# Performance work log

Hardware: AMD Instinct MI355X
Metric: run time of the kernel (lower is better)

## Reference

```python
import jax, jax.numpy as jnp
import numpy as np

MODES = (16, 16, 16)  # (kx, ky, kz); rfft keeps kz//2+1 = 9 modes on last axis


def setup_inputs() -> dict:
    key = jax.random.key(0)
    k_x, k_w1, k_w2 = jax.random.split(key, 3)
    B, C, H, W, D = 4, 64, 64, 64, 64
    hidden = C // 4
    kzr = MODES[2] // 2 + 1
    gate_dim = MODES[0] * MODES[1] * kzr  # 16*16*9 = 2304
    x = jax.random.normal(k_x, (B, C, H, W, D), dtype=jnp.float32)
    w1 = jax.random.normal(k_w1, (C, hidden), dtype=jnp.float32) * (1.0 / np.sqrt(C))
    b1 = jnp.zeros((hidden,), dtype=jnp.float32)
    w2 = jax.random.normal(k_w2, (hidden, gate_dim), dtype=jnp.float32) * (1.0 / np.sqrt(hidden))
    b2 = jnp.zeros((gate_dim,), dtype=jnp.float32)
    return {"x": x, "w1": w1, "b1": b1, "w2": w2, "b2": b2}


def reference(x, w1, b1, w2, b2):
    B = x.shape[0]
    kx, ky, kz = MODES
    kzr = kz // 2 + 1
    # Gate network: global average pool over spatial dims -> MLP -> sigmoid
    pooled = jnp.mean(x, axis=(2, 3, 4))                      # [B, C]
    h = jax.nn.relu(pooled @ w1 + b1)                          # [B, C//4]
    gates = jax.nn.sigmoid(h @ w2 + b2)                        # [B, kx*ky*kzr]
    gates = gates.reshape(B, 1, kx, ky, kzr)                   # broadcast over channels
    # Full 3D rFFT, gate only the low-frequency corner block, inverse FFT
    x_ft = jnp.fft.rfftn(x, axes=(-3, -2, -1))                 # [B, C, H, W, D//2+1] complex
    x_ft_gated = x_ft.at[:, :, :kx, :ky, :kzr].multiply(gates.astype(x_ft.real.dtype))
    out = jnp.fft.irfftn(x_ft_gated, s=x.shape[-3:], axes=(-3, -2, -1))
    return out.astype(x.dtype)
```

## Files before the change

kernel.cpp:

```cpp
#include <hip/hip_runtime.h>

namespace {

typedef float f2 __attribute__((ext_vector_type(2)));
typedef float vf4 __attribute__((ext_vector_type(4)));

__device__ __forceinline__ f2 mkf2(float a, float b) { f2 r; r.x = a; r.y = b; return r; }
__device__ __forceinline__ f2 pkfma(float s, f2 b, f2 c) {
  return __builtin_elementwise_fma(mkf2(s, s), b, c);
}

constexpr float COS64[64] = {
  1.00000000f,  0.99518473f,  0.98078528f,  0.95694034f,
  0.92387953f,  0.88192126f,  0.83146961f,  0.77301045f,
  0.70710678f,  0.63439328f,  0.55557023f,  0.47139674f,
  0.38268343f,  0.29028468f,  0.19509032f,  0.09801714f,
  0.00000000f, -0.09801714f, -0.19509032f, -0.29028468f,
 -0.38268343f, -0.47139674f, -0.55557023f, -0.63439328f,
 -0.70710678f, -0.77301045f, -0.83146961f, -0.88192126f,
 -0.92387953f, -0.95694034f, -0.98078528f, -0.99518473f,
 -1.00000000f, -0.99518473f, -0.98078528f, -0.95694034f,
 -0.92387953f, -0.88192126f, -0.83146961f, -0.77301045f,
 -0.70710678f, -0.63439328f, -0.55557023f, -0.47139674f,
 -0.38268343f, -0.29028468f, -0.19509032f, -0.09801714f,
 -0.00000000f,  0.09801714f,  0.19509032f,  0.29028468f,
  0.38268343f,  0.47139674f,  0.55557023f,  0.63439328f,
  0.70710678f,  0.77301045f,  0.83146961f,  0.88192126f,
  0.92387953f,  0.95694034f,  0.98078528f,  0.99518473f };

constexpr int MM = 144;
constexpr int GD = 2304;

__device__ __forceinline__ void rot_mi(int m, float r_in, float i_in,
                                       float& r_out, float& i_out) {
  float r  = (m & 1) ? i_in : r_in;
  float i2 = (m & 1) ? r_in : i_in;
  r  = (m >= 2) ? -r : r;
  i2 = (m == 1 || m == 2) ? -i2 : i2;
  r_out = r; i_out = i2;
}

__global__ __launch_bounds__(256) void k1_fwd(const float* __restrict__ x,
                                              float2* __restrict__ buf1) {
  __shared__ float xs[64 * 68];
  __shared__ float2 As[9 * 67];
  const int tid = threadIdx.x;
  const int slice = blockIdx.x;
  const int w = tid >> 2, q = tid & 3;

  const float4* xp = (const float4*)(x + ((size_t)slice << 12));
  const float4 a0 = xp[tid];
  const float4 a1 = xp[tid + 256];
  const float4 a2 = xp[tid + 512];
  const float4 a3 = xp[tid + 768];
  {
    const int s0 = tid & 15, hi = tid >> 4;
    *(float4*)&xs[(hi +  0) * 68 + s0 * 4] = a0;
    *(float4*)&xs[(hi + 16) * 68 + s0 * 4] = a1;
    *(float4*)&xs[(hi + 32) * 68 + s0 * 4] = a2;
    *(float4*)&xs[(hi + 48) * 68 + s0 * 4] = a3;
  }
  __syncthreads();

  float xv[16];
  {
    const float4 b0 = *(const float4*)&xs[w * 68 + q * 16 + 0];
    const float4 b1 = *(const float4*)&xs[w * 68 + q * 16 + 4];
    const float4 b2 = *(const float4*)&xs[w * 68 + q * 16 + 8];
    const float4 b3 = *(const float4*)&xs[w * 68 + q * 16 + 12];
    xv[0]=b0.x; xv[1]=b0.y; xv[2]=b0.z; xv[3]=b0.w;
    xv[4]=b1.x; xv[5]=b1.y; xv[6]=b1.z; xv[7]=b1.w;
    xv[8]=b2.x; xv[9]=b2.y; xv[10]=b2.z; xv[11]=b2.w;
    xv[12]=b3.x; xv[13]=b3.y; xv[14]=b3.z; xv[15]=b3.w;
  }

  f2 A[9];
#pragma unroll
  for (int kz = 0; kz < 9; ++kz) A[kz] = mkf2(0.f, 0.f);
#pragma unroll
  for (int j = 0; j < 16; ++j) {
    const float v = xv[j];
#pragma unroll
    for (int kz = 0; kz < 9; ++kz) {
      const int n = (kz * j) & 63;
      A[kz] = pkfma(v, mkf2(COS64[n], -COS64[(n + 48) & 63]), A[kz]);
    }
  }
#pragma unroll
  for (int kz = 0; kz < 9; ++kz) {
    const int m = (q * kz) & 3;
    float r, i2;
    rot_mi(m, A[kz].x, A[kz].y, r, i2);
    r  += __shfl_xor(r, 1);  r  += __shfl_xor(r, 2);
    i2 += __shfl_xor(i2, 1); i2 += __shfl_xor(i2, 2);
    if (q == 0) As[kz * 67 + w] = make_float2(r, i2);
  }
  __syncthreads();

  if (tid < MM) {
    const int ky = tid / 9, kz = tid - ky * 9;
    const float cs = COS64[ky], sn = COS64[(ky + 48) & 63];
    const int m1 = ky & 3, m2 = (2 * ky) & 3, m3 = (3 * ky) & 3;
    float px = 1.f, py = 0.f, br = 0.f, bi = 0.f;
    const float2* Ak = As + kz * 67;
#pragma unroll
    for (int b = 0; b < 16; ++b) {
      const float2 v0 = Ak[b];
      const float2 v1 = Ak[b + 16];
      const float2 v2 = Ak[b + 32];
      const float2 v3 = Ak[b + 48];
      float gr = v0.x, gi = v0.y, rr, ri;
      rot_mi(m1, v1.x, v1.y, rr, ri); gr += rr; gi += ri;
      rot_mi(m2, v2.x, v2.y, rr, ri); gr += rr; gi += ri;
      rot_mi(m3, v3.x, v3.y, rr, ri); gr += rr; gi += ri;
      br = fmaf(gr, px, fmaf(-gi, py, br));
      bi = fmaf(gr, py, fmaf( gi, px, bi));
      const float nx = fmaf(px, cs,  py * sn);
      const float ny = fmaf(py, cs, -px * sn);
      px = nx; py = ny;
    }
    buf1[(size_t)slice * MM + tid] = make_float2(br, bi);
  }
}

__global__ __launch_bounds__(256) void k3_gates(const float2* __restrict__ buf1,
    const float* __restrict__ w1, const float* __restrict__ b1,
    const float* __restrict__ w2, const float* __restrict__ b2,
    float* __restrict__ gm1) {
  __shared__ float pooled[64];
  __shared__ float hs[16];
  const int b = blockIdx.x, tid = threadIdx.x;
  const int c = tid >> 2, q = tid & 3;
  {
    const float2* bp = buf1 + ((size_t)((b * 64 + c) * 64) + q) * MM;
    float s = 0.f;
    for (int t = 0; t < 16; ++t) s += bp[(size_t)t * 4 * MM].x;
    s += __shfl_xor(s, 1); s += __shfl_xor(s, 2);
    if (q == 0) pooled[c] = s * (1.f / 262144.f);
  }
  __syncthreads();
  if (tid < 16) {
    float acc = b1[tid];
    for (int cc = 0; cc < 64; ++cc) acc = fmaf(pooled[cc], w1[cc * 16 + tid], acc);
    hs[tid] = fmaxf(acc, 0.f);
  }
  __syncthreads();
#pragma unroll
  for (int r = 0; r < 9; ++r) {
    const int o = tid + r * 256;
    float acc = b2[o];
#pragma unroll
    for (int j = 0; j < 16; ++j) acc = fmaf(hs[j], w2[j * GD + o], acc);
    gm1[b * GD + o] = 1.f / (1.f + expf(-acc)) - 1.f;
  }
}

__global__ __launch_bounds__(256) void k2_fwd(const float2* __restrict__ buf1,
                                              const float* __restrict__ gm1,
                                              float2* __restrict__ C1buf) {
  __shared__ float2 Bs[32 * MM];
  __shared__ float2 Dg[GD];
  __shared__ float2 rotS[64 * 16];
  const int tid = threadIdx.x, bc = blockIdx.x, b = bc >> 6;
  const int kx = tid >> 4, g = tid & 15;

#pragma unroll
  for (int u = 0; u < 4; ++u) {
    const int e = tid * 4 + u, hh = e >> 4, kxx = e & 15;
    const int n = (kxx * hh) & 63;
    rotS[e] = make_float2(COS64[n], COS64[(n + 48) & 63]);
  }

  float accR[9], accI[9];
#pragma unroll
  for (int j = 0; j < 9; ++j) { accR[j] = 0.f; accI[j] = 0.f; }
  float qR = 1.f, qI = 0.f;
  const float hc = COS64[kx], hsn = COS64[(kx + 48) & 63];

  const float4* src = (const float4*)(buf1 + (size_t)bc * 64 * MM);
  for (int c2 = 0; c2 < 2; ++c2) {
    float4* dst4 = (float4*)Bs;
    for (int i = tid; i < 2304; i += 256) dst4[i] = src[c2 * 2304 + i];
    __syncthreads();
    for (int hh = 0; hh < 32; ++hh) {
      const float2* row = Bs + hh * MM + g * 9;
#pragma unroll
      for (int j = 0; j < 9; ++j) {
        const float2 bv = row[j];
        accR[j] = fmaf(bv.x, qR, fmaf(-bv.y, qI, accR[j]));
        accI[j] = fmaf(bv.x, qI, fmaf( bv.y, qR, accI[j]));
      }
      const float nR = fmaf(qR, hc, qI * hsn);
      const float nI = fmaf(qI, hc, -qR * hsn);
      qR = nR; qI = nI;
    }
    __syncthreads();
  }

  {
    const float* gp = gm1 + (size_t)b * GD + kx * MM + g * 9;
    float2* dp = Dg + kx * MM + g * 9;
#pragma unroll
    for (int j = 0; j < 9; ++j) {
      const float gg = gp[j];
      dp[j] = make_float2(accR[j] * gg, accI[j] * gg);
    }
  }
  __syncthreads();

  {
    const int h = tid >> 2, mq = tid & 3;
    float2* dst = C1buf + ((size_t)(bc * 64 + h)) * MM + mq * 36;
    for (int jb = 0; jb < 3; ++jb) {
      float aR[12], aI[12];
#pragma unroll
      for (int j = 0; j < 12; ++j) { aR[j] = 0.f; aI[j] = 0.f; }
      for (int kxx = 0; kxx < 16; ++kxx) {
        const float2 rot = rotS[h * 16 + kxx];
        const float2* drow = Dg + kxx * MM + mq * 36 + jb * 12;
#pragma unroll
        for (int j = 0; j < 12; ++j) {
          const float2 d = drow[j];
          aR[j] = fmaf(d.x, rot.x, fmaf(-d.y, rot.y, aR[j]));
          aI[j] = fmaf(d.x, rot.y, fmaf( d.y, rot.x, aI[j]));
        }
      }
#pragma unroll
      for (int j = 0; j < 12; ++j) dst[jb * 12 + j] = make_float2(aR[j], aI[j]);
    }
  }
}

__global__ __launch_bounds__(256) void k4b_final(const float2* __restrict__ C1buf,
                                                 const float* __restrict__ x,
                                                 float* __restrict__ out) {
  __shared__ float2 C1s[MM];
  __shared__ float2 C2s[9 * 65];
  __shared__ float deltaS[64 * 68];
  const int tid = threadIdx.x;
  const int slice = 16383 - blockIdx.x;
  const int w = tid >> 2, q = tid & 3;

  const float4* xp = (const float4*)(x + ((size_t)slice << 12));
  const float4 xv0 = xp[tid];
  const float4 xv1 = xp[tid + 256];
  const float4 xv2 = xp[tid + 512];
  const float4 xv3 = xp[tid + 768];

  if (tid < 72) {
    const float4* cp = (const float4*)(C1buf + (size_t)slice * MM);
    ((float4*)C1s)[tid] = cp[tid];
  }
  __syncthreads();

  {
    const float cs = COS64[w], sn = COS64[(w + 48) & 63];
    const int kz0 = q, kz1 = q + 4;
    f2 A0 = mkf2(0.f, 0.f), A1 = mkf2(0.f, 0.f), A2 = mkf2(0.f, 0.f);
    f2 P = mkf2(1.f, 0.f);
    for (int ky = 0; ky < 16; ++ky) {
      const f2 Pn = mkf2(-P.y, P.x);
      const float2 c0 = C1s[ky * 9 + kz0];
      const float2 c1 = C1s[ky * 9 + kz1];
      A0 = pkfma(c0.x, P, A0);  A0 = pkfma(c0.y, Pn, A0);
      A1 = pkfma(c1.x, P, A1);  A1 = pkfma(c1.y, Pn, A1);
      if (q == 0) {
        const float2 c2v = C1s[ky * 9 + 8];
        A2 = pkfma(c2v.x, P, A2);  A2 = pkfma(c2v.y, Pn, A2);
      }
      P = pkfma(sn, Pn, cs * P);
    }
    const float scale = 1.f / 262144.f;
    C2s[kz0 * 65 + w] = make_float2(A0.x * scale, A0.y * scale);
    C2s[kz1 * 65 + w] = make_float2(A1.x * scale, A1.y * scale);
    if (q == 0) C2s[8 * 65 + w] = make_float2(A2.x * scale, A2.y * scale);
  }
  __syncthreads();

  {
    float cr[9], ci[9];
#pragma unroll
    for (int kz = 0; kz < 9; ++kz) {
      const float2 v = C2s[kz * 65 + w];
      const int m = (kz * q) & 3;
      const float a = v.x, b2_ = v.y;
      float r  = (m & 1) ? b2_ : a;
      float i2 = (m & 1) ? a : b2_;
      r  = (m == 1 || m == 2) ? -r : r;
      i2 = (m >= 2) ? -i2 : i2;
      cr[kz] = r; ci[kz] = i2;
    }
    f2 acc2[8];
#pragma unroll
    for (int p = 0; p < 8; ++p) acc2[p] = mkf2(cr[0], cr[0]);
#pragma unroll
    for (int kz = 1; kz < 9; ++kz) {
#pragma unroll
      for (int p = 0; p < 8; ++p) {
        const int n0 = (kz * (2 * p)) & 63, n1 = (kz * (2 * p + 1)) & 63;
        acc2[p] = pkfma(cr[kz],
                        mkf2(2.f * COS64[n0], 2.f * COS64[n1]), acc2[p]);
        acc2[p] = pkfma(ci[kz],
                        mkf2(-2.f * COS64[(n0 + 48) & 63],
                             -2.f * COS64[(n1 + 48) & 63]), acc2[p]);
      }
    }
    float* ds = &deltaS[w * 68 + q * 16];
#pragma unroll
    for (int p = 0; p < 8; ++p) {
      ds[2 * p]     = acc2[p].x;
      ds[2 * p + 1] = acc2[p].y;
    }
  }
  __syncthreads();

  {
    const int s0 = tid & 15, hi = tid >> 4;
    const float4 r0 = *(const float4*)&deltaS[(hi +  0) * 68 + s0 * 4];
    const float4 r1 = *(const float4*)&deltaS[(hi + 16) * 68 + s0 * 4];
    const float4 r2 = *(const float4*)&deltaS[(hi + 32) * 68 + s0 * 4];
    const float4 r3 = *(const float4*)&deltaS[(hi + 48) * 68 + s0 * 4];
    vf4* op = (vf4*)(out + ((size_t)slice << 12));
    vf4 o0, o1, o2, o3;
    o0.x = xv0.x + r0.x; o0.y = xv0.y + r0.y; o0.z = xv0.z + r0.z; o0.w = xv0.w + r0.w;
    o1.x = xv1.x + r1.x; o1.y = xv1.y + r1.y; o1.z = xv1.z + r1.z; o1.w = xv1.w + r1.w;
    o2.x = xv2.x + r2.x; o2.y = xv2.y + r2.y; o2.z = xv2.z + r2.z; o2.w = xv2.w + r2.w;
    o3.x = xv3.x + r3.x; o3.y = xv3.y + r3.y; o3.z = xv3.z + r3.z; o3.w = xv3.w + r3.w;
    __builtin_nontemporal_store(o0, &op[tid]);
    __builtin_nontemporal_store(o1, &op[tid + 256]);
    __builtin_nontemporal_store(o2, &op[tid + 512]);
    __builtin_nontemporal_store(o3, &op[tid + 768]);
  }
}

}

extern "C" void kernel_launch(void* const* d_in, const int* in_sizes, int n_in,
                              void* d_out, int out_size, void* d_ws, size_t ws_size,
                              hipStream_t stream) {
  (void)in_sizes; (void)n_in; (void)out_size; (void)ws_size;
  const float* x  = (const float*)d_in[0];
  const float* w1 = (const float*)d_in[1];
  const float* b1 = (const float*)d_in[2];
  const float* w2 = (const float*)d_in[3];
  const float* b2 = (const float*)d_in[4];
  float* out = (float*)d_out;

  char* ws = (char*)d_ws;
  float2* buf1  = (float2*)ws;
  float*  gm1   = (float*)(ws + 18874368);
  float2* c1buf = (float2*)(ws + 18911232);

  hipLaunchKernelGGL(k1_fwd,   dim3(16384),    dim3(256), 0, stream, x, buf1);
  hipLaunchKernelGGL(k3_gates, dim3(4),        dim3(256), 0, stream, buf1, w1, b1, w2, b2, gm1);
  hipLaunchKernelGGL(k2_fwd,   dim3(256),      dim3(256), 0, stream, buf1, gm1, c1buf);
  hipLaunchKernelGGL(k4b_final,dim3(16384),    dim3(256), 0, stream, c1buf, x, out);
}
```

Baseline: 232.6 us.

## Fuse gate MLP into k2 and process two slices per k1 block with prefetch

The small gate kernel is folded into k2_fwd. Each of the 256 blocks now recomputes the pooled mean, the MLP and the sigmoid gates for its batch and keeps them in shared memory, which removes one launch and the gm1 global round trip. k1_fwd now handles two slices per block and prefetches the second slice's input while the first is computed, halving the grid. The price is redundant gate computation in every k2 block (64 blocks per batch re-read buf1 and w2) and more shared memory per block, which may lower occupancy.

```diff
diff --git a/kernel.cpp b/kernel.cpp
--- a/kernel.cpp
+++ b/kernel.cpp
@@ -45,93 +45,112 @@
   __shared__ float xs[64 * 68];
   __shared__ float2 As[9 * 67];
   const int tid = threadIdx.x;
-  const int slice = blockIdx.x;
+  const int slice0 = blockIdx.x * 2;
   const int w = tid >> 2, q = tid & 3;
-
-  const float4* xp = (const float4*)(x + ((size_t)slice << 12));
-  const float4 a0 = xp[tid];
-  const float4 a1 = xp[tid + 256];
-  const float4 a2 = xp[tid + 512];
-  const float4 a3 = xp[tid + 768];
-  {
-    const int s0 = tid & 15, hi = tid >> 4;
+  const int s0 = tid & 15, hi = tid >> 4;
+
+  const float4* xp0 = (const float4*)(x + ((size_t)slice0 << 12));
+  float4 a0 = xp0[tid];
+  float4 a1 = xp0[tid + 256];
+  float4 a2 = xp0[tid + 512];
+  float4 a3 = xp0[tid + 768];
+  float4 b0, b1, b2, b3;
+
+  for (int s = 0; s < 2; ++s) {
     *(float4*)&xs[(hi +  0) * 68 + s0 * 4] = a0;
     *(float4*)&xs[(hi + 16) * 68 + s0 * 4] = a1;
     *(float4*)&xs[(hi + 32) * 68 + s0 * 4] = a2;
     *(float4*)&xs[(hi + 48) * 68 + s0 * 4] = a3;
-  }
-  __syncthreads();
-
-  float xv[16];
-  {
-    const float4 b0 = *(const float4*)&xs[w * 68 + q * 16 + 0];
-    const float4 b1 = *(const float4*)&xs[w * 68 + q * 16 + 4];
-    const float4 b2 = *(const float4*)&xs[w * 68 + q * 16 + 8];
-    const float4 b3 = *(const float4*)&xs[w * 68 + q * 16 + 12];
-    xv[0]=b0.x; xv[1]=b0.y; xv[2]=b0.z; xv[3]=b0.w;
-    xv[4]=b1.x; xv[5]=b1.y; xv[6]=b1.z; xv[7]=b1.w;
-    xv[8]=b2.x; xv[9]=b2.y; xv[10]=b2.z; xv[11]=b2.w;
-    xv[12]=b3.x; xv[13]=b3.y; xv[14]=b3.z; xv[15]=b3.w;
-  }
-
-  f2 A[9];
-#pragma unroll
-  for (int kz = 0; kz < 9; ++kz) A[kz] = mkf2(0.f, 0.f);
-#pragma unroll
-  for (int j = 0; j < 16; ++j) {
-    const float v = xv[j];
+    if (s == 0) {
+      const float4* xp1 = (const float4*)(x + ((size_t)(slice0 + 1) << 12));
+      b0 = xp1[tid];
+      b1 = xp1[tid + 256];
+      b2 = xp1[tid + 512];
+      b3 = xp1[tid + 768];
+    }
+    __syncthreads();
+
+    float xv[16];
+    {
+      const float4 c0 = *(const float4*)&xs[w * 68 + q * 16 + 0];
+      const float4 c1 = *(const float4*)&xs[w * 68 + q * 16 + 4];
+      const float4 c2 = *(const float4*)&xs[w * 68 + q * 16 + 8];
+      const float4 c3 = *(const float4*)&xs[w * 68 + q * 16 + 12];
+      xv[0]=c0.x; xv[1]=c0.y; xv[2]=c0.z; xv[3]=c0.w;
+      xv[4]=c1.x; xv[5]=c1.y; xv[6]=c1.z; xv[7]=c1.w;
+      xv[8]=c2.x; xv[9]=c2.y; xv[10]=c2.z; xv[11]=c2.w;
+      xv[12]=c3.x; xv[13]=c3.y; xv[14]=c3.z; xv[15]=c3.w;
+    }
+
+    f2 A[9];
+#pragma unroll
+    for (int kz = 0; kz < 9; ++kz) A[kz] = mkf2(0.f, 0.f);
+#pragma unroll
+    for (int j = 0; j < 16; ++j) {
+      const float v = xv[j];
+#pragma unroll
+      for (int kz = 0; kz < 9; ++kz) {
+        const int n = (kz * j) & 63;
+        A[kz] = pkfma(v, mkf2(COS64[n], -COS64[(n + 48) & 63]), A[kz]);
+      }
+    }
 #pragma unroll
     for (int kz = 0; kz < 9; ++kz) {
-      const int n = (kz * j) & 63;
-      A[kz] = pkfma(v, mkf2(COS64[n], -COS64[(n + 48) & 63]), A[kz]);
-    }
-  }
-#pragma unroll
-  for (int kz = 0; kz < 9; ++kz) {
-    const int m = (q * kz) & 3;
-    float r, i2;
-    rot_mi(m, A[kz].x, A[kz].y, r, i2);
-    r  += __shfl_xor(r, 1);  r  += __shfl_xor(r, 2);
-    i2 += __shfl_xor(i2, 1); i2 += __shfl_xor(i2, 2);
-    if (q == 0) As[kz * 67 + w] = make_float2(r, i2);
-  }
-  __syncthreads();
-
-  if (tid < MM) {
-    const int ky = tid / 9, kz = tid - ky * 9;
-    const float cs = COS64[ky], sn = COS64[(ky + 48) & 63];
-    const int m1 = ky & 3, m2 = (2 * ky) & 3, m3 = (3 * ky) & 3;
-    float px = 1.f, py = 0.f, br = 0.f, bi = 0.f;
-    const float2* Ak = As + kz * 67;
-#pragma unroll
-    for (int b = 0; b < 16; ++b) {
-      const float2 v0 = Ak[b];
-      const float2 v1 = Ak[b + 16];
-      const float2 v2 = Ak[b + 32];
-      const float2 v3 = Ak[b + 48];
-      float gr = v0.x, gi = v0.y, rr, ri;
-      rot_mi(m1, v1.x, v1.y, rr, ri); gr += rr; gi += ri;
-      rot_mi(m2, v2.x, v2.y, rr, ri); gr += rr; gi += ri;
-      rot_mi(m3, v3.x, v3.y, rr, ri); gr += rr; gi += ri;
-      br = fmaf(gr, px, fmaf(-gi, py, br));
-      bi = fmaf(gr, py, fmaf( gi, px, bi));
-      const float nx = fmaf(px, cs,  py * sn);
-      const float ny = fmaf(py, cs, -px * sn);
-      px = nx; py = ny;
-    }
-    buf1[(size_t)slice * MM + tid] = make_float2(br, bi);
-  }
-}
-
-__global__ __launch_bounds__(256) void k3_gates(const float2* __restrict__ buf1,
+      const int m = (q * kz) & 3;
+      float r, i2;
+      rot_mi(m, A[kz].x, A[kz].y, r, i2);
+      r  += __shfl_xor(r, 1);  r  += __shfl_xor(r, 2);
+      i2 += __shfl_xor(i2, 1); i2 += __shfl_xor(i2, 2);
+      if (q == 0) As[kz * 67 + w] = make_float2(r, i2);
+    }
+    __syncthreads();
+
+    if (tid < MM) {
+      const int ky = tid / 9, kz = tid - ky * 9;
+      const float cs = COS64[ky], sn = COS64[(ky + 48) & 63];
+      const int m1 = ky & 3, m2 = (2 * ky) & 3, m3 = (3 * ky) & 3;
+      float px = 1.f, py = 0.f, br = 0.f, bi = 0.f;
+      const float2* Ak = As + kz * 67;
+#pragma unroll
+      for (int b = 0; b < 16; ++b) {
+        const float2 v0 = Ak[b];
+        const float2 v1 = Ak[b + 16];
+        const float2 v2 = Ak[b + 32];
+        const float2 v3 = Ak[b + 48];
+        float gr = v0.x, gi = v0.y, rr, ri;
+        rot_mi(m1, v1.x, v1.y, rr, ri); gr += rr; gi += ri;
+        rot_mi(m2, v2.x, v2.y, rr, ri); gr += rr; gi += ri;
+        rot_mi(m3, v3.x, v3.y, rr, ri); gr += rr; gi += ri;
+        br = fmaf(gr, px, fmaf(-gi, py, br));
+        bi = fmaf(gr, py, fmaf( gi, px, bi));
+        const float nx = fmaf(px, cs,  py * sn);
+        const float ny = fmaf(py, cs, -px * sn);
+        px = nx; py = ny;
+      }
+      buf1[(size_t)(slice0 + s) * MM + tid] = make_float2(br, bi);
+    }
+    if (s == 0) {
+      __syncthreads();
+      a0 = b0; a1 = b1; a2 = b2; a3 = b3;
+    }
+  }
+}
+
+__global__ __launch_bounds__(256) void k2_fwd(const float2* __restrict__ buf1,
     const float* __restrict__ w1, const float* __restrict__ b1,
     const float* __restrict__ w2, const float* __restrict__ b2,
-    float* __restrict__ gm1) {
+    float2* __restrict__ C1buf) {
+  __shared__ float2 Bs[32 * MM];
+  __shared__ float2 Dg[GD];
+  __shared__ float2 rotS[64 * 16];
+  __shared__ float gS[GD];
   __shared__ float pooled[64];
   __shared__ float hs[16];
-  const int b = blockIdx.x, tid = threadIdx.x;
-  const int c = tid >> 2, q = tid & 3;
-  {
+  const int tid = threadIdx.x, bc = blockIdx.x, b = bc >> 6;
+  const int kx = tid >> 4, g = tid & 15;
+
+  {
+    const int c = tid >> 2, q = tid & 3;
     const float2* bp = buf1 + ((size_t)((b * 64 + c) * 64) + q) * MM;
     float s = 0.f;
     for (int t = 0; t < 16; ++t) s += bp[(size_t)t * 4 * MM].x;
@@ -151,18 +170,8 @@
     float acc = b2[o];
 #pragma unroll
     for (int j = 0; j < 16; ++j) acc = fmaf(hs[j], w2[j * GD + o], acc);
-    gm1[b * GD + o] = 1.f / (1.f + expf(-acc)) - 1.f;
-  }
-}
-
-__global__ __launch_bounds__(256) void k2_fwd(const float2* __restrict__ buf1,
-                                              const float* __restrict__ gm1,
-                                              float2* __restrict__ C1buf) {
-  __shared__ float2 Bs[32 * MM];
-  __shared__ float2 Dg[GD];
-  __shared__ float2 rotS[64 * 16];
-  const int tid = threadIdx.x, bc = blockIdx.x, b = bc >> 6;
-  const int kx = tid >> 4, g = tid & 15;
+    gS[o] = 1.f / (1.f + expf(-acc)) - 1.f;
+  }
 
 #pragma unroll
   for (int u = 0; u < 4; ++u) {
@@ -198,7 +207,7 @@
   }
 
   {
-    const float* gp = gm1 + (size_t)b * GD + kx * MM + g * 9;
+    const float* gp = gS + kx * MM + g * 9;
     float2* dp = Dg + kx * MM + g * 9;
 #pragma unroll
     for (int j = 0; j < 9; ++j) {
@@ -348,11 +357,9 @@
 
   char* ws = (char*)d_ws;
   float2* buf1  = (float2*)ws;
-  float*  gm1   = (float*)(ws + 18874368);
-  float2* c1buf = (float2*)(ws + 18911232);
-
-  hipLaunchKernelGGL(k1_fwd,   dim3(16384),    dim3(256), 0, stream, x, buf1);
-  hipLaunchKernelGGL(k3_gates, dim3(4),        dim3(256), 0, stream, buf1, w1, b1, w2, b2, gm1);
-  hipLaunchKernelGGL(k2_fwd,   dim3(256),      dim3(256), 0, stream, buf1, gm1, c1buf);
+  float2* c1buf = (float2*)(ws + 18874368);
+
+  hipLaunchKernelGGL(k1_fwd,   dim3(8192),     dim3(256), 0, stream, x, buf1);
+  hipLaunchKernelGGL(k2_fwd,   dim3(256),      dim3(256), 0, stream, buf1, w1, b1, w2, b2, c1buf);
   hipLaunchKernelGGL(k4b_final,dim3(16384),    dim3(256), 0, stream, c1buf, x, out);
 }
```

Result: faster. 212.9 us (-8.5%).
